# Kernel optimization log

Measured on AMD Instinct MI355X. Metric: run time of the kernel, lower is better.

## Reference

```python
import jax, jax.numpy as jnp
import numpy as np

B, S, D = 4, 2048, 1024
H, DK, DV = 16, 64, 64

def setup_inputs() -> dict:
    key = jax.random.key(0)
    ks = jax.random.split(key, 8)
    def xavier(k, fan_in, fan_out):
        limit = float(np.sqrt(6.0 / (fan_in + fan_out)))
        return jax.random.uniform(k, (fan_in, fan_out), jnp.float32, -limit, limit)
    return {
        "Q": jax.random.normal(ks[0], (B, S, D), jnp.float32),
        "K": jax.random.normal(ks[1], (B, S, D), jnp.float32),
        "V": jax.random.normal(ks[2], (B, S, D), jnp.float32),
        "mask": jax.random.uniform(ks[3], (B, S), jnp.float32),
        "Wq": xavier(ks[4], D, H * DK),  # stored [in, out]; torch Linear applies x @ W.T
        "bq": jnp.zeros((H * DK,), jnp.float32),
        "Wk": xavier(ks[5], D, H * DK),
        "bk": jnp.zeros((H * DK,), jnp.float32),
        "Wv": xavier(ks[6], D, H * DV),
        "bv": jnp.zeros((H * DV,), jnp.float32),
    }

def reference(Q, K, V, mask, Wq, bq, Wk, bk, Wv, bv):
    b, s, _ = Q.shape
    # projections -> [b, h, s, d]
    q = (Q @ Wq + bq).reshape(b, s, H, DK).transpose(0, 2, 1, 3)
    k = (K @ Wk + bk).reshape(b, s, H, DK).transpose(0, 2, 1, 3)
    v = (V @ Wv + bv).reshape(b, s, H, DV).transpose(0, 2, 1, 3)
    scores = jnp.einsum('bhqd,bhkd->bhqk', q, k) / jnp.sqrt(jnp.float32(DK))
    e = jnp.exp(scores)  # NOTE: raw exp, no max-subtraction (faithful to source)
    e = e * mask[:, None, None, :]  # multiplicative mask over key dim
    attn = e / (jnp.sum(e, axis=-1, keepdims=True) + 1e-8)
    context = jnp.einsum('bhqk,bhkd->bhqd', attn, v)
    return context.transpose(0, 2, 1, 3).reshape(b, s, H * DV)
```

## Files before the change

### kernel.cpp

```cpp
#include <hip/hip_runtime.h>
#include <hip/hip_bf16.h>
#include <stdint.h>

typedef short bf16x8 __attribute__((ext_vector_type(8)));
typedef float f32x4 __attribute__((ext_vector_type(4)));
typedef unsigned int u32x2 __attribute__((ext_vector_type(2)));
typedef unsigned int u32x4 __attribute__((ext_vector_type(4)));

__device__ __forceinline__ unsigned short f2bf(float f) {
  union { float f; unsigned u; } x; x.f = f;
  unsigned r = x.u + 0x7FFFu + ((x.u >> 16) & 1u);
  return (unsigned short)(r >> 16);
}

__device__ __forceinline__ unsigned pk2bf(float a, float b) {
  union { __hip_bfloat162 h; unsigned u; } x;
  x.h = __float22bfloat162_rn(make_float2(a, b));
  return x.u;
}

typedef const __attribute__((address_space(1))) unsigned int* gptr_t;
typedef __attribute__((address_space(3))) unsigned int* lptr_t;
__device__ __forceinline__ void gll16(const void* g, void* l) {
  __builtin_amdgcn_global_load_lds((gptr_t)g, (lptr_t)l, 16, 0, 0);
}

__global__ __launch_bounds__(1024) void wt_kernel(const float* __restrict__ Wq,
                                                  const float* __restrict__ Wk,
                                                  const float* __restrict__ Wv,
                                                  unsigned short* __restrict__ wt) {
  const float* W = blockIdx.z == 0 ? Wq : (blockIdx.z == 1 ? Wk : Wv);
  unsigned short* o = wt + (size_t)blockIdx.z * 1048576;
  __shared__ float t[32][33];
  int tx = threadIdx.x, ty = threadIdx.y;
  t[ty][tx] = W[(size_t)(blockIdx.y * 32 + ty) * 1024 + blockIdx.x * 32 + tx];
  __syncthreads();
  o[(size_t)(blockIdx.x * 32 + ty) * 1024 + blockIdx.y * 32 + tx] = f2bf(t[tx][ty]);
}

__global__ __launch_bounds__(256) void cvt_kernel(const float* __restrict__ Q,
                                                  const float* __restrict__ K,
                                                  const float* __restrict__ V,
                                                  unsigned short* __restrict__ out) {
  int y = blockIdx.y;
  const float* s = y == 0 ? Q : (y == 1 ? K : V);
  unsigned short* o = out + (size_t)y * 8388608;
  size_t idx = ((size_t)blockIdx.x * 256 + threadIdx.x) * 8;
  float4 f0 = *(const float4*)(s + idx);
  float4 f1 = *(const float4*)(s + idx + 4);
  u32x4 r = {pk2bf(f0.x, f0.y), pk2bf(f0.z, f0.w), pk2bf(f1.x, f1.y), pk2bf(f1.z, f1.w)};
  *(u32x4*)(o + idx) = r;
}

__global__ __launch_bounds__(256) void proj_kernel(
    const unsigned short* __restrict__ Xb, const unsigned short* __restrict__ wt,
    const float* __restrict__ bq, const float* __restrict__ bk, const float* __restrict__ bv,
    unsigned short* __restrict__ qo, unsigned short* __restrict__ ko, unsigned short* __restrict__ vo) {
  int p = blockIdx.z;
  const unsigned short* X = Xb + (size_t)p * 8388608;
  const unsigned short* Wt = wt + (size_t)p * 1048576;
  const float* bias = p == 0 ? bq : (p == 1 ? bk : bv);
  unsigned short* out = p == 0 ? qo : (p == 1 ? ko : vo);

  __shared__ __align__(16) unsigned short abuf[8192];
  __shared__ __align__(16) unsigned short bbuf[8192];

  int tid = threadIdx.x;
  int lane = tid & 63, w = tid >> 6;
  int l15 = lane & 15, quad = lane >> 4;
  int wm = w >> 1, wn = w & 1;
  int m0 = blockIdx.x * 128, n0 = blockIdx.y * 128;

  f32x4 acc[4][4] = {};

  for (int kk = 0; kk < 16; ++kk) {
    int k0 = kk * 64;
    for (int j = 0; j < 4; ++j) {
      int stj = w * 4 + j;
      int kt = stj >> 3, t = stj & 7;
      gll16(Wt + (size_t)(n0 + t * 16 + l15) * 1024 + k0 + kt * 32 + quad * 8, &bbuf[stj * 512]);
      gll16(X + (size_t)(m0 + t * 16 + l15) * 1024 + k0 + kt * 32 + quad * 8, &abuf[stj * 512]);
    }
    __syncthreads();
    for (int kt = 0; kt < 2; ++kt) {
      bf16x8 af[4], bfr[4];
      for (int i = 0; i < 4; ++i) af[i]  = *(const bf16x8*)&abuf[(kt * 8 + wm * 4 + i) * 512 + lane * 8];
      for (int j = 0; j < 4; ++j) bfr[j] = *(const bf16x8*)&bbuf[(kt * 8 + wn * 4 + j) * 512 + lane * 8];
      for (int i = 0; i < 4; ++i)
        for (int j = 0; j < 4; ++j)
          acc[i][j] = __builtin_amdgcn_mfma_f32_16x16x32_bf16(af[i], bfr[j], acc[i][j], 0, 0, 0);
    }
    __syncthreads();
  }

  bool isv = (p == 2);
  for (int j = 0; j < 4; ++j) {
    int n = n0 + wn * 64 + j * 16 + l15;
    float bl = bias[n];
    int h = n >> 6, d = n & 63;
    for (int i = 0; i < 4; ++i) {
      for (int r = 0; r < 4; ++r) {
        int m = m0 + wm * 64 + i * 16 + quad * 4 + r;
        int b = m >> 11, s = m & 2047;
        float val = acc[i][j][r] + bl;
        size_t idx;
        if (isv) idx = ((size_t)((b * 16 + h) * 64 + d) << 11) + s;
        else     idx = ((size_t)((b * 16 + h) * 2048 + s) << 6) + d;
        out[idx] = f2bf(val);
      }
    }
  }
}

__global__ __launch_bounds__(256, 3) void attn_kernel(
    const unsigned short* __restrict__ q, const unsigned short* __restrict__ k,
    const unsigned short* __restrict__ vT, const float* __restrict__ mask,
    float* __restrict__ out) {
  int qb = blockIdx.x, h = blockIdx.y, b = blockIdx.z;
  int tid = threadIdx.x, lane = tid & 63, w = tid >> 6;
  int l15 = lane & 15, quad = lane >> 4;

  __shared__ __align__(16) unsigned short un[16384];
  __shared__ __align__(16) unsigned short vls[8192];

  const unsigned short* qp = q + (size_t)(b * 16 + h) * 2048 * 64;
  const unsigned short* kp = k + (size_t)(b * 16 + h) * 2048 * 64;
  const unsigned short* vp = vT + (size_t)(b * 16 + h) * 64 * 2048;
  const float* mp = mask + (size_t)b * 2048;

  bf16x8 aq[2][2];
  for (int nt = 0; nt < 2; ++nt)
    for (int kt = 0; kt < 2; ++kt)
      aq[nt][kt] = *(const bf16x8*)(qp + (size_t)(qb * 128 + w * 32 + nt * 16 + l15) * 64 + kt * 32 + quad * 8);

  f32x4 oacc[2][4] = {};
  f32x4 dacc[2] = {};
  bf16x8 ones = {0x3F80, 0x3F80, 0x3F80, 0x3F80, 0x3F80, 0x3F80, 0x3F80, 0x3F80};

  unsigned short* pw = &un[w * 4096];

  for (int kb = 0; kb < 16; ++kb) {
    int kbase = kb * 128;
    for (int j = 0; j < 4; ++j) {
      int stj = w * 4 + j;
      int kt = stj >> 3, t = stj & 7;
      gll16(kp + (size_t)(kbase + t * 16 + l15) * 64 + kt * 32 + quad * 8, &un[stj * 512]);
      int kt2 = stj >> 2, t2 = stj & 3;
      gll16(vp + (size_t)(t2 * 16 + l15) * 2048 + kbase + kt2 * 32 + quad * 8, &vls[stj * 512]);
    }
    __syncthreads();

    f32x4 sacc[8][2] = {};
    for (int mt16 = 0; mt16 < 8; ++mt16)
      for (int kt = 0; kt < 2; ++kt) {
        bf16x8 ak = *(const bf16x8*)&un[(kt * 8 + mt16) * 512 + lane * 8];
        sacc[mt16][0] = __builtin_amdgcn_mfma_f32_16x16x32_bf16(ak, aq[0][kt], sacc[mt16][0], 0, 0, 0);
        sacc[mt16][1] = __builtin_amdgcn_mfma_f32_16x16x32_bf16(ak, aq[1][kt], sacc[mt16][1], 0, 0, 0);
      }

    __syncthreads();

    for (int mt16 = 0; mt16 < 8; ++mt16) {
      float4 mv = *(const float4*)&mp[kbase + mt16 * 16 + quad * 4];
      const float* mm = (const float*)&mv;
      for (int nt = 0; nt < 2; ++nt) {
        float e0 = __expf(sacc[mt16][nt][0] * 0.125f) * mm[0];
        float e1 = __expf(sacc[mt16][nt][1] * 0.125f) * mm[1];
        float e2 = __expf(sacc[mt16][nt][2] * 0.125f) * mm[2];
        float e3 = __expf(sacc[mt16][nt][3] * 0.125f) * mm[3];
        u32x2 wv = {pk2bf(e0, e1), pk2bf(e2, e3)};
        *(u32x2*)&pw[(nt * 8 + mt16) * 256 + lane * 4] = wv;
      }
    }

    for (int kt = 0; kt < 4; ++kt) {
      int t = kt * 2 + (quad >> 1);
      int srcl = ((quad & 1) * 2) * 16 + l15;
      bf16x8 pa[2];
      for (int mt = 0; mt < 2; ++mt) {
        union { u32x2 p[2]; bf16x8 v; } u;
        int base = (mt * 8 + t) * 256 + srcl * 4;
        u.p[0] = *(const u32x2*)&pw[base];
        u.p[1] = *(const u32x2*)&pw[base + 64];
        pa[mt] = u.v;
      }
      dacc[0] = __builtin_amdgcn_mfma_f32_16x16x32_bf16(pa[0], ones, dacc[0], 0, 0, 0);
      dacc[1] = __builtin_amdgcn_mfma_f32_16x16x32_bf16(pa[1], ones, dacc[1], 0, 0, 0);
      for (int nt = 0; nt < 4; ++nt) {
        bf16x8 bv = *(const bf16x8*)&vls[(kt * 4 + nt) * 512 + lane * 8];
        oacc[0][nt] = __builtin_amdgcn_mfma_f32_16x16x32_bf16(pa[0], bv, oacc[0][nt], 0, 0, 0);
        oacc[1][nt] = __builtin_amdgcn_mfma_f32_16x16x32_bf16(pa[1], bv, oacc[1][nt], 0, 0, 0);
      }
    }
    __syncthreads();
  }

  for (int mt = 0; mt < 2; ++mt)
    for (int r = 0; r < 4; ++r) {
      int s = qb * 128 + w * 32 + mt * 16 + quad * 4 + r;
      float rden = 1.0f / (dacc[mt][r] + 1e-8f);
      for (int nt = 0; nt < 4; ++nt) {
        int dv = nt * 16 + l15;
        out[(size_t)(b * 2048 + s) * 1024 + h * 64 + dv] = oacc[mt][nt][r] * rden;
      }
    }
}

extern "C" void kernel_launch(void* const* d_in, const int* in_sizes, int n_in,
                              void* d_out, int out_size, void* d_ws, size_t ws_size,
                              hipStream_t stream) {
  const float* Q    = (const float*)d_in[0];
  const float* K    = (const float*)d_in[1];
  const float* V    = (const float*)d_in[2];
  const float* mask = (const float*)d_in[3];
  const float* Wq   = (const float*)d_in[4];
  const float* bq   = (const float*)d_in[5];
  const float* Wk   = (const float*)d_in[6];
  const float* bk   = (const float*)d_in[7];
  const float* Wv   = (const float*)d_in[8];
  const float* bv   = (const float*)d_in[9];

  char* ws = (char*)d_ws;
  unsigned short* wt = (unsigned short*)ws;
  unsigned short* qb = (unsigned short*)(ws + 6291456);
  unsigned short* kb = (unsigned short*)(ws + 23068672);
  unsigned short* vb = (unsigned short*)(ws + 39845888);
  unsigned short* xb = (unsigned short*)(ws + 56623104);

  hipLaunchKernelGGL(wt_kernel, dim3(32, 32, 3), dim3(32, 32), 0, stream, Wq, Wk, Wv, wt);
  hipLaunchKernelGGL(cvt_kernel, dim3(4096, 3), dim3(256), 0, stream, Q, K, V, xb);
  hipLaunchKernelGGL(proj_kernel, dim3(64, 8, 3), dim3(256), 0, stream,
                     xb, wt, bq, bk, bv, qb, kb, vb);
  hipLaunchKernelGGL(attn_kernel, dim3(16, 16, 4), dim3(256), 0, stream,
                     qb, kb, vb, mask, (float*)d_out);
}
```

Baseline: 436.4 us.

## Keep softmax probabilities in registers via transposed MFMA and coalesce output stores

Restructures the attention inner loop so that scores are computed as K·Q^T and fed straight into 16x16x16 MFMAs as the B operand. This avoids the LDS round-trip for the probability matrix and removes one barrier per key block. LDS shrinks to a single shared K/V buffer, occupancy hint rises to 4 blocks, exp uses exp2 with a folded constant, and the epilogue stages output through LDS for float4 coalesced writes. The risks are more, smaller MFMA instructions and narrower V LDS reads.

```diff
diff --git a/kernel.cpp b/kernel.cpp
--- a/kernel.cpp
+++ b/kernel.cpp
@@ -3,6 +3,7 @@
 #include <stdint.h>
 
 typedef short bf16x8 __attribute__((ext_vector_type(8)));
+typedef short bf16x4 __attribute__((ext_vector_type(4)));
 typedef float f32x4 __attribute__((ext_vector_type(4)));
 typedef unsigned int u32x2 __attribute__((ext_vector_type(2)));
 typedef unsigned int u32x4 __attribute__((ext_vector_type(4)));
@@ -112,7 +113,7 @@
   }
 }
 
-__global__ __launch_bounds__(256, 3) void attn_kernel(
+__global__ __launch_bounds__(256, 4) void attn_kernel(
     const unsigned short* __restrict__ q, const unsigned short* __restrict__ k,
     const unsigned short* __restrict__ vT, const float* __restrict__ mask,
     float* __restrict__ out) {
@@ -120,8 +121,9 @@
   int tid = threadIdx.x, lane = tid & 63, w = tid >> 6;
   int l15 = lane & 15, quad = lane >> 4;
 
-  __shared__ __align__(16) unsigned short un[16384];
-  __shared__ __align__(16) unsigned short vls[8192];
+  __shared__ __align__(16) unsigned short smem[16384];
+  unsigned short* kls = smem;
+  unsigned short* vls = smem + 8192;
 
   const unsigned short* qp = q + (size_t)(b * 16 + h) * 2048 * 64;
   const unsigned short* kp = k + (size_t)(b * 16 + h) * 2048 * 64;
@@ -135,75 +137,67 @@
 
   f32x4 oacc[2][4] = {};
   f32x4 dacc[2] = {};
-  bf16x8 ones = {0x3F80, 0x3F80, 0x3F80, 0x3F80, 0x3F80, 0x3F80, 0x3F80, 0x3F80};
-
-  unsigned short* pw = &un[w * 4096];
+  bf16x4 ones4 = {0x3F80, 0x3F80, 0x3F80, 0x3F80};
+
+  const float expc = 0.18033688011112042f;
+  int srclA = ((quad >> 1)) * 16 + l15;
+  int voff = (quad & 1) * 4;
 
   for (int kb = 0; kb < 16; ++kb) {
     int kbase = kb * 128;
+    __syncthreads();
     for (int j = 0; j < 4; ++j) {
       int stj = w * 4 + j;
       int kt = stj >> 3, t = stj & 7;
-      gll16(kp + (size_t)(kbase + t * 16 + l15) * 64 + kt * 32 + quad * 8, &un[stj * 512]);
+      gll16(kp + (size_t)(kbase + t * 16 + l15) * 64 + kt * 32 + quad * 8, &kls[stj * 512]);
       int kt2 = stj >> 2, t2 = stj & 3;
       gll16(vp + (size_t)(t2 * 16 + l15) * 2048 + kbase + kt2 * 32 + quad * 8, &vls[stj * 512]);
     }
     __syncthreads();
 
-    f32x4 sacc[8][2] = {};
-    for (int mt16 = 0; mt16 < 8; ++mt16)
+    for (int t = 0; t < 8; ++t) {
+      f32x4 s0 = {}, s1 = {};
       for (int kt = 0; kt < 2; ++kt) {
-        bf16x8 ak = *(const bf16x8*)&un[(kt * 8 + mt16) * 512 + lane * 8];
-        sacc[mt16][0] = __builtin_amdgcn_mfma_f32_16x16x32_bf16(ak, aq[0][kt], sacc[mt16][0], 0, 0, 0);
-        sacc[mt16][1] = __builtin_amdgcn_mfma_f32_16x16x32_bf16(ak, aq[1][kt], sacc[mt16][1], 0, 0, 0);
+        bf16x8 ak = *(const bf16x8*)&kls[(kt * 8 + t) * 512 + lane * 8];
+        s0 = __builtin_amdgcn_mfma_f32_16x16x32_bf16(ak, aq[0][kt], s0, 0, 0, 0);
+        s1 = __builtin_amdgcn_mfma_f32_16x16x32_bf16(ak, aq[1][kt], s1, 0, 0, 0);
       }
-
-    __syncthreads();
-
-    for (int mt16 = 0; mt16 < 8; ++mt16) {
-      float4 mv = *(const float4*)&mp[kbase + mt16 * 16 + quad * 4];
-      const float* mm = (const float*)&mv;
-      for (int nt = 0; nt < 2; ++nt) {
-        float e0 = __expf(sacc[mt16][nt][0] * 0.125f) * mm[0];
-        float e1 = __expf(sacc[mt16][nt][1] * 0.125f) * mm[1];
-        float e2 = __expf(sacc[mt16][nt][2] * 0.125f) * mm[2];
-        float e3 = __expf(sacc[mt16][nt][3] * 0.125f) * mm[3];
-        u32x2 wv = {pk2bf(e0, e1), pk2bf(e2, e3)};
-        *(u32x2*)&pw[(nt * 8 + mt16) * 256 + lane * 4] = wv;
+      float4 mv = *(const float4*)&mp[kbase + t * 16 + quad * 4];
+      float e00 = exp2f(s0[0] * expc) * mv.x, e01 = exp2f(s0[1] * expc) * mv.y;
+      float e02 = exp2f(s0[2] * expc) * mv.z, e03 = exp2f(s0[3] * expc) * mv.w;
+      float e10 = exp2f(s1[0] * expc) * mv.x, e11 = exp2f(s1[1] * expc) * mv.y;
+      float e12 = exp2f(s1[2] * expc) * mv.z, e13 = exp2f(s1[3] * expc) * mv.w;
+      union { u32x2 u; bf16x4 v; } p0, p1;
+      p0.u = (u32x2){pk2bf(e00, e01), pk2bf(e02, e03)};
+      p1.u = (u32x2){pk2bf(e10, e11), pk2bf(e12, e13)};
+
+      dacc[0] = __builtin_amdgcn_mfma_f32_16x16x16bf16_1k(ones4, p0.v, dacc[0], 0, 0, 0);
+      dacc[1] = __builtin_amdgcn_mfma_f32_16x16x16bf16_1k(ones4, p1.v, dacc[1], 0, 0, 0);
+
+      int vbase = (t >> 1) * 2048 + ((t & 1) * 32 + srclA) * 8 + voff;
+      for (int dvt = 0; dvt < 4; ++dvt) {
+        bf16x4 av = *(const bf16x4*)&vls[vbase + dvt * 512];
+        oacc[0][dvt] = __builtin_amdgcn_mfma_f32_16x16x16bf16_1k(av, p0.v, oacc[0][dvt], 0, 0, 0);
+        oacc[1][dvt] = __builtin_amdgcn_mfma_f32_16x16x16bf16_1k(av, p1.v, oacc[1][dvt], 0, 0, 0);
       }
     }
-
-    for (int kt = 0; kt < 4; ++kt) {
-      int t = kt * 2 + (quad >> 1);
-      int srcl = ((quad & 1) * 2) * 16 + l15;
-      bf16x8 pa[2];
-      for (int mt = 0; mt < 2; ++mt) {
-        union { u32x2 p[2]; bf16x8 v; } u;
-        int base = (mt * 8 + t) * 256 + srcl * 4;
-        u.p[0] = *(const u32x2*)&pw[base];
-        u.p[1] = *(const u32x2*)&pw[base + 64];
-        pa[mt] = u.v;
-      }
-      dacc[0] = __builtin_amdgcn_mfma_f32_16x16x32_bf16(pa[0], ones, dacc[0], 0, 0, 0);
-      dacc[1] = __builtin_amdgcn_mfma_f32_16x16x32_bf16(pa[1], ones, dacc[1], 0, 0, 0);
-      for (int nt = 0; nt < 4; ++nt) {
-        bf16x8 bv = *(const bf16x8*)&vls[(kt * 4 + nt) * 512 + lane * 8];
-        oacc[0][nt] = __builtin_amdgcn_mfma_f32_16x16x32_bf16(pa[0], bv, oacc[0][nt], 0, 0, 0);
-        oacc[1][nt] = __builtin_amdgcn_mfma_f32_16x16x32_bf16(pa[1], bv, oacc[1][nt], 0, 0, 0);
-      }
-    }
-    __syncthreads();
-  }
-
-  for (int mt = 0; mt < 2; ++mt)
-    for (int r = 0; r < 4; ++r) {
-      int s = qb * 128 + w * 32 + mt * 16 + quad * 4 + r;
-      float rden = 1.0f / (dacc[mt][r] + 1e-8f);
-      for (int nt = 0; nt < 4; ++nt) {
-        int dv = nt * 16 + l15;
-        out[(size_t)(b * 2048 + s) * 1024 + h * 64 + dv] = oacc[mt][nt][r] * rden;
-      }
-    }
+  }
+
+  float* eb = (float*)smem;
+  float* ew = eb + w * 1040;
+  for (int mt = 0; mt < 2; ++mt) {
+    __syncthreads();
+    float rden = 1.0f / (dacc[mt][0] + 1e-8f);
+    for (int dvt = 0; dvt < 4; ++dvt)
+      for (int r = 0; r < 4; ++r)
+        ew[l15 * 65 + dvt * 16 + quad * 4 + r] = oacc[mt][dvt][r] * rden;
+    __syncthreads();
+    int row = lane >> 2, seg = lane & 3;
+    const float* src = &ew[row * 65 + seg * 16];
+    float* op = out + (size_t)(b * 2048 + qb * 128 + w * 32 + mt * 16 + row) * 1024 + h * 64 + seg * 16;
+    for (int i = 0; i < 4; ++i)
+      *(float4*)(op + i * 4) = *(const float4*)(src + i * 4);
+  }
 }
 
 extern "C" void kernel_launch(void* const* d_in, const int* in_sizes, int n_in,
```

After: 443.0 us. About the same (+1.5%).
